# Optimization experiments

Hardware: AMD Instinct MI355X
Metric: run time of the kernel (lower is better)

## Reference

```python
import jax, jax.numpy as jnp
import numpy as np

N = 100000
E = 1600000
NFEAT = 256
NCLASS = 40
H1, C1 = 8, 8  # layer1: 8 heads x 8 channels, concat -> 64
EPS = 1e-16
NEG_SLOPE = 0.2


def setup_inputs() -> dict:
    key = jax.random.key(0)
    ks = jax.random.split(key, 10)
    x = jax.random.normal(ks[0], (N, NFEAT), dtype=jnp.float32)
    # random edges with no self-loops (PyG GATConv removes then re-adds self loops)
    src = jax.random.randint(ks[1], (E,), 0, N)
    off = jax.random.randint(ks[2], (E,), 1, N)
    dst = (src + off) % N
    edge_index = jnp.stack([src, dst]).astype(jnp.int64)
    glorot = lambda k, shp, fan: jax.random.uniform(k, shp, jnp.float32, -1.0, 1.0) * np.sqrt(6.0 / fan)
    # layer 1: in=256 -> heads=8, out=8
    W1 = glorot(ks[3], (NFEAT, H1 * C1), NFEAT + H1 * C1)
    att_src1 = glorot(ks[4], (H1, C1), 2 * C1)
    att_dst1 = glorot(ks[5], (H1, C1), 2 * C1)
    b1 = jnp.zeros((H1 * C1,), jnp.float32)
    # layer 2: in=64 -> heads=1, out=nclass
    W2 = glorot(ks[6], (H1 * C1, NCLASS), H1 * C1 + NCLASS)
    att_src2 = glorot(ks[7], (1, NCLASS), 2 * NCLASS)
    att_dst2 = glorot(ks[8], (1, NCLASS), 2 * NCLASS)
    b2 = jnp.zeros((NCLASS,), jnp.float32)
    return {"x": x, "edge_index": edge_index, "W1": W1, "att_src1": att_src1,
            "att_dst1": att_dst1, "b1": b1, "W2": W2, "att_src2": att_src2,
            "att_dst2": att_dst2, "b2": b2}


def gat_conv(x, src, dst, W, att_src, att_dst, bias, heads, out_ch):
    n = x.shape[0]
    h = (x @ W).reshape(n, heads, out_ch)               # [N,H,C]
    a_src = (h * att_src[None]).sum(-1)                  # [N,H]
    a_dst = (h * att_dst[None]).sum(-1)                  # [N,H]
    e = jax.nn.leaky_relu(a_src[src] + a_dst[dst], NEG_SLOPE)  # [E,H]
    # segment softmax over incoming edges of each target node
    m = jax.ops.segment_max(e, dst, num_segments=n)
    e = jnp.exp(e - m[dst])
    s = jax.ops.segment_sum(e, dst, num_segments=n)
    alpha = e / (s[dst] + EPS)                           # [E,H]
    msg = h[src] * alpha[..., None]                      # [E,H,C]
    out = jax.ops.segment_sum(msg, dst, num_segments=n)  # [N,H,C]
    return out.reshape(n, heads * out_ch) + bias


def reference(x, edge_index, W1, att_src1, att_dst1, b1, W2, att_src2, att_dst2, b2):
    # add self loops (PyG GATConv default add_self_loops=True)
    loops = jnp.arange(N, dtype=edge_index.dtype)
    src = jnp.concatenate([edge_index[0], loops])
    dst = jnp.concatenate([edge_index[1], loops])
    h = gat_conv(x, src, dst, W1, att_src1, att_dst1, b1, H1, C1)  # [N,64]
    h = jax.nn.elu(h)
    out = gat_conv(h, src, dst, W2, att_src2, att_dst2, b2, 1, NCLASS)  # [N,nclass]
    return out
```

## Files before the change

kernel.cpp:

```cpp
#include <hip/hip_runtime.h>
#include <hip/hip_bf16.h>

#define NN 100000
#define NE 1600000
#define NF 256
#define NC 40
#define NH 8
#define D1 64
#define NEG 0.2f
#define BSHIFT 7
#define BSZ 128
#define NB ((NN + BSZ - 1) / BSZ)
#define EPB 4096
#define NBLK ((NE + EPB - 1) / EPB)

typedef __attribute__((ext_vector_type(8))) short short8;
typedef __attribute__((ext_vector_type(4))) float f32x4;

static __device__ __forceinline__ float lrelu(float x) { return x > 0.f ? x : NEG * x; }

static __device__ __forceinline__ float2 bfx2(unsigned u) {
    union { unsigned q; float f; } a, b;
    a.q = u << 16;
    b.q = u & 0xFFFF0000u;
    return make_float2(a.f, b.f);
}

static __device__ __forceinline__ unsigned packbf2(float x, float y) {
    unsigned xu = __float_as_uint(x), yu = __float_as_uint(y);
    xu = (xu + 0x7FFFu + ((xu >> 16) & 1u)) >> 16;
    yu = (yu + 0x7FFFu + ((yu >> 16) & 1u)) >> 16;
    return xu | (yu << 16);
}

static __device__ __forceinline__ unsigned short f2b(float x) {
    unsigned u = __float_as_uint(x);
    u = (u + 0x7FFFu + ((u >> 16) & 1u)) >> 16;
    return (unsigned short)u;
}


__launch_bounds__(256)
__global__ void bhist_k(const int* __restrict__ dst, int* __restrict__ cnt) {
    __shared__ int hist[NB];
    int i = blockIdx.x, t = threadIdx.x;
    for (int b = t; b < NB; b += 256) hist[b] = 0;
    __syncthreads();
    int e0 = i * EPB;
    #pragma unroll
    for (int k = 0; k < EPB / 256; ++k) {
        int e = e0 + k * 256 + t;
        if (e < NE) atomicAdd(&hist[dst[e] >> BSHIFT], 1);
    }
    __syncthreads();
    for (int b = t; b < NB; b += 256) cnt[i * NB + b] = hist[b];
}

__launch_bounds__(256)
__global__ void bscan2_k(int* __restrict__ cnt, int* __restrict__ btot) {
    __shared__ int ps[256];
    int b = blockIdx.x, t = threadIdx.x;
    int i0 = 2 * t;
    int a = (i0 < NBLK) ? cnt[i0 * NB + b] : 0;
    int c = (i0 + 1 < NBLK) ? cnt[(i0 + 1) * NB + b] : 0;
    int s = a + c;
    ps[t] = s;
    __syncthreads();
    #pragma unroll
    for (int off = 1; off < 256; off <<= 1) {
        int x = (t >= off) ? ps[t - off] : 0;
        __syncthreads();
        ps[t] += x;
        __syncthreads();
    }
    int ex = ps[t] - s;
    if (i0 < NBLK) cnt[i0 * NB + b] = ex;
    if (i0 + 1 < NBLK) cnt[(i0 + 1) * NB + b] = ex + a;
    if (t == 255) btot[b] = ps[255];
}

__launch_bounds__(256)
__global__ void bscanB_k(const int* __restrict__ btot, int* __restrict__ bbase) {
    __shared__ int ps[256];
    int t = threadIdx.x;
    int j0 = 4 * t;
    int v[4]; int s = 0;
    #pragma unroll
    for (int k = 0; k < 4; ++k) { v[k] = (j0 + k < NB) ? btot[j0 + k] : 0; s += v[k]; }
    ps[t] = s;
    __syncthreads();
    #pragma unroll
    for (int off = 1; off < 256; off <<= 1) {
        int x = (t >= off) ? ps[t - off] : 0;
        __syncthreads();
        ps[t] += x;
        __syncthreads();
    }
    int run = ps[t] - s;
    #pragma unroll
    for (int k = 0; k < 4; ++k) { if (j0 + k < NB) bbase[j0 + k] = run; run += v[k]; }
    if (t == 0) bbase[NB] = NE;
}

__launch_bounds__(256)
__global__ void bplace_k(const int* __restrict__ src, const int* __restrict__ dst,
                         const int* __restrict__ cnt, const int* __restrict__ bbase,
                         long long* __restrict__ tmp) {
    __shared__ int loff[NB];
    int i = blockIdx.x, t = threadIdx.x;
    for (int b = t; b < NB; b += 256) loff[b] = bbase[b] + cnt[i * NB + b];
    __syncthreads();
    int e0 = i * EPB;
    #pragma unroll
    for (int k = 0; k < EPB / 256; ++k) {
        int e = e0 + k * 256 + t;
        if (e < NE) {
            int d = dst[e];
            int p = atomicAdd(&loff[d >> BSHIFT], 1);
            tmp[p] = ((long long)d << 32) | (unsigned)src[e];
        }
    }
}

__launch_bounds__(256)
__global__ void scatter2_k(const long long* __restrict__ tmp, const int* __restrict__ bbase,
                           int* __restrict__ rowptr, int* __restrict__ col) {
    __shared__ int lcnt[BSZ];
    __shared__ int lrow[BSZ];
    __shared__ int ls[BSZ];
    int b = blockIdx.x, t = threadIdx.x;
    int n0 = b << BSHIFT;
    if (t < BSZ) lcnt[t] = 0;
    __syncthreads();
    int beg = bbase[b], end = bbase[b + 1];
    for (int p = beg + t; p < end; p += 256) {
        int d = (int)(tmp[p] >> 32);
        atomicAdd(&lcnt[d - n0], 1);
    }
    __syncthreads();
    if (t < BSZ) ls[t] = lcnt[t];
    __syncthreads();
    #pragma unroll
    for (int off = 1; off < BSZ; off <<= 1) {
        int x = 0;
        if (t < BSZ && t >= off) x = ls[t - off];
        __syncthreads();
        if (t < BSZ) ls[t] += x;
        __syncthreads();
    }
    if (t < BSZ) {
        int ex = ls[t] - lcnt[t];
        lrow[t] = beg + ex;
        if (n0 + t < NN) rowptr[n0 + t] = beg + ex;
        lcnt[t] = 0;
    }
    if (b == NB - 1 && t == 0) rowptr[NN] = NE;
    __syncthreads();
    for (int p = beg + t; p < end; p += 256) {
        long long v = tmp[p];
        int d = (int)(v >> 32);
        int s = (int)(v & 0xFFFFFFFFLL);
        int o = atomicAdd(&lcnt[d - n0], 1);
        col[lrow[d - n0] + o] = s;
    }
}


__launch_bounds__(256)
__global__ void gemm1_k(const float* __restrict__ x, const float* __restrict__ W,
                        unsigned short* __restrict__ h1b) {
    __shared__ unsigned short wsw[8 * 4 * 64 * 8];
    int tid = threadIdx.x;
    int wid = tid >> 6, lane = tid & 63;
    int r0 = blockIdx.x * 128 + wid * 32;

    #pragma unroll
    for (int it = 0; it < 16; ++it) {
        int idx4 = it * 256 + tid;
        int k = idx4 >> 4;
        int c0 = (idx4 & 15) * 4;
        float4 v = *(const float4*)&W[k * 64 + c0];
        int kt = k >> 5, kg = (k >> 3) & 3, kr = k & 7;
        float vv[4] = {v.x, v.y, v.z, v.w};
        #pragma unroll
        for (int j = 0; j < 4; ++j) {
            int c = c0 + j;
            int dest = (((kt * 4 + (c >> 4)) * 64) + kg * 16 + (c & 15)) * 8 + kr;
            wsw[dest] = f2b(vv[j]);
        }
    }
    __syncthreads();

    int arow0 = r0 + (lane & 15);
    int kg8 = (lane >> 4) * 8;
    f32x4 acc[2][4] = {};
    for (int kt = 0; kt < 8; ++kt) {
        short8 af[2];
        #pragma unroll
        for (int rt = 0; rt < 2; ++rt) {
            int row = arow0 + rt * 16;
            float4 v0 = make_float4(0.f, 0.f, 0.f, 0.f), v1 = v0;
            if (row < NN) {
                const float* px = &x[row * NF + kt * 32 + kg8];
                v0 = *(const float4*)px;
                v1 = *(const float4*)(px + 4);
            }
            unsigned p0 = packbf2(v0.x, v0.y), p1 = packbf2(v0.z, v0.w);
            unsigned p2 = packbf2(v1.x, v1.y), p3 = packbf2(v1.z, v1.w);
            af[rt][0] = (short)(p0 & 0xFFFF); af[rt][1] = (short)(p0 >> 16);
            af[rt][2] = (short)(p1 & 0xFFFF); af[rt][3] = (short)(p1 >> 16);
            af[rt][4] = (short)(p2 & 0xFFFF); af[rt][5] = (short)(p2 >> 16);
            af[rt][6] = (short)(p3 & 0xFFFF); af[rt][7] = (short)(p3 >> 16);
        }
        #pragma unroll
        for (int ct = 0; ct < 4; ++ct) {
            short8 bf = *(const short8*)&wsw[((kt * 4 + ct) * 64 + lane) * 8];
            acc[0][ct] = __builtin_amdgcn_mfma_f32_16x16x32_bf16(af[0], bf, acc[0][ct], 0, 0, 0);
            acc[1][ct] = __builtin_amdgcn_mfma_f32_16x16x32_bf16(af[1], bf, acc[1][ct], 0, 0, 0);
        }
    }

    int ccol = lane & 15;
    int crow0 = r0 + (lane >> 4) * 4;
    #pragma unroll
    for (int rt = 0; rt < 2; ++rt) {
        #pragma unroll
        for (int r = 0; r < 4; ++r) {
            int grow = crow0 + rt * 16 + r;
            if (grow < NN) {
                #pragma unroll
                for (int ct = 0; ct < 4; ++ct)
                    h1b[grow * D1 + ct * 16 + ccol] = f2b(acc[rt][ct][r]);
            }
        }
    }
}


__global__ void attn1_k(const unsigned short* __restrict__ h1b, const float* __restrict__ asrc,
                        const float* __restrict__ adst,
                        float* __restrict__ as1, float* __restrict__ ad1) {
    int t = blockIdx.x * blockDim.x + threadIdx.x;
    if (t >= NN * NH) return;
    int n = t >> 3, h = t & 7;
    uint4 v = *(const uint4*)&h1b[n * D1 + h * 8];
    float hv[8];
    float2 p;
    p = bfx2(v.x); hv[0] = p.x; hv[1] = p.y;
    p = bfx2(v.y); hv[2] = p.x; hv[3] = p.y;
    p = bfx2(v.z); hv[4] = p.x; hv[5] = p.y;
    p = bfx2(v.w); hv[6] = p.x; hv[7] = p.y;
    float sa = 0.f, sd = 0.f;
    #pragma unroll
    for (int c = 0; c < 8; ++c) {
        sa = fmaf(hv[c], asrc[h * 8 + c], sa);
        sd = fmaf(hv[c], adst[h * 8 + c], sd);
    }
    as1[t] = sa;
    ad1[t] = sd;
}


__launch_bounds__(256)
__global__ void agg1_k(const unsigned short* __restrict__ h1b, const float* __restrict__ as1,
                       const float* __restrict__ ad1,
                       const int* __restrict__ rowptr, const int* __restrict__ col,
                       const float* __restrict__ b1, unsigned short* __restrict__ h1outb) {
    int n = blockIdx.x * 4 + (threadIdx.x >> 6);
    if (n >= NN) return;
    int lane = threadIdx.x & 63;
    int g = lane >> 3, ln = lane & 7;
    int row0 = rowptr[n];
    int d = rowptr[n + 1] - row0;
    float adh = ad1[n * 8 + ln];

    float acc[8] = {};
    float wsum = 0.f;
    for (int j = 0; j <= d; j += 8) {
        int jj = j + g;
        int s = (jj < d) ? col[row0 + jj] : n;
        float e = lrelu(as1[s * 8 + ln] + adh);
        float wgt = (jj <= d) ? __expf(e) : 0.f;
        wsum += wgt;
        uint4 hv = *(const uint4*)&h1b[s * D1 + ln * 8];
        float2 p;
        p = bfx2(hv.x); acc[0] = fmaf(p.x, wgt, acc[0]); acc[1] = fmaf(p.y, wgt, acc[1]);
        p = bfx2(hv.y); acc[2] = fmaf(p.x, wgt, acc[2]); acc[3] = fmaf(p.y, wgt, acc[3]);
        p = bfx2(hv.z); acc[4] = fmaf(p.x, wgt, acc[4]); acc[5] = fmaf(p.y, wgt, acc[5]);
        p = bfx2(hv.w); acc[6] = fmaf(p.x, wgt, acc[6]); acc[7] = fmaf(p.y, wgt, acc[7]);
    }
    #pragma unroll
    for (int off = 8; off <= 32; off <<= 1) {
        wsum += __shfl_xor(wsum, off, 64);
        #pragma unroll
        for (int k = 0; k < 8; ++k) acc[k] += __shfl_xor(acc[k], off, 64);
    }
    if (g == 0) {
        float inv = 1.f / (wsum + 1e-16f);
        unsigned u[4];
        #pragma unroll
        for (int k = 0; k < 4; ++k) {
            float v0 = fmaf(acc[2 * k], inv, b1[ln * 8 + 2 * k]);
            float v1 = fmaf(acc[2 * k + 1], inv, b1[ln * 8 + 2 * k + 1]);
            v0 = (v0 > 0.f) ? v0 : (__expf(v0) - 1.f);
            v1 = (v1 > 0.f) ? v1 : (__expf(v1) - 1.f);
            u[k] = packbf2(v0, v1);
        }
        uint4 w = {u[0], u[1], u[2], u[3]};
        *(uint4*)&h1outb[n * D1 + ln * 8] = w;
    }
}


__launch_bounds__(256)
__global__ void attn2_k(const unsigned short* __restrict__ h1outb, const float* __restrict__ W2,
                        const float* __restrict__ asrc, const float* __restrict__ adst,
                        float* __restrict__ as2, float* __restrict__ ad2) {
    __shared__ float w2a[64], w2d[64];
    int tid = threadIdx.x;
    if (tid < 128) {
        int c = tid & 63;
        const float* av = (tid < 64) ? asrc : adst;
        float s = 0.f;
        #pragma unroll
        for (int j = 0; j < NC; ++j) s = fmaf(W2[c * NC + j], av[j], s);
        if (tid < 64) w2a[c] = s; else w2d[c] = s;
    }
    __syncthreads();
    int n = blockIdx.x * 256 + tid;
    if (n >= NN) return;
    float sa = 0.f, sd = 0.f;
    #pragma unroll
    for (int q = 0; q < 8; ++q) {
        uint4 v = *(const uint4*)&h1outb[n * D1 + q * 8];
        int c0 = q * 8;
        float2 p;
        p = bfx2(v.x);
        sa = fmaf(p.x, w2a[c0], sa);     sd = fmaf(p.x, w2d[c0], sd);
        sa = fmaf(p.y, w2a[c0 + 1], sa); sd = fmaf(p.y, w2d[c0 + 1], sd);
        p = bfx2(v.y);
        sa = fmaf(p.x, w2a[c0 + 2], sa); sd = fmaf(p.x, w2d[c0 + 2], sd);
        sa = fmaf(p.y, w2a[c0 + 3], sa); sd = fmaf(p.y, w2d[c0 + 3], sd);
        p = bfx2(v.z);
        sa = fmaf(p.x, w2a[c0 + 4], sa); sd = fmaf(p.x, w2d[c0 + 4], sd);
        sa = fmaf(p.y, w2a[c0 + 5], sa); sd = fmaf(p.y, w2d[c0 + 5], sd);
        p = bfx2(v.w);
        sa = fmaf(p.x, w2a[c0 + 6], sa); sd = fmaf(p.x, w2d[c0 + 6], sd);
        sa = fmaf(p.y, w2a[c0 + 7], sa); sd = fmaf(p.y, w2d[c0 + 7], sd);
    }
    as2[n] = sa;
    ad2[n] = sd;
}


__launch_bounds__(256)
__global__ void agg2_k(const unsigned short* __restrict__ h1outb, const float* __restrict__ as2,
                       const float* __restrict__ ad2,
                       const int* __restrict__ rowptr, const int* __restrict__ col,
                       unsigned short* __restrict__ zb) {
    int n = blockIdx.x * 4 + (threadIdx.x >> 6);
    if (n >= NN) return;
    int lane = threadIdx.x & 63;
    int g = lane >> 3, ln = lane & 7;
    int row0 = rowptr[n];
    int d = rowptr[n + 1] - row0;
    float adn = ad2[n];

    float acc[8] = {};
    float wsum = 0.f;
    for (int j = 0; j <= d; j += 8) {
        int jj = j + g;
        int s = (jj < d) ? col[row0 + jj] : n;
        float e = lrelu(as2[s] + adn);
        float wgt = (jj <= d) ? __expf(e) : 0.f;
        wsum += wgt;
        uint4 hv = *(const uint4*)&h1outb[s * D1 + ln * 8];
        float2 p;
        p = bfx2(hv.x); acc[0] = fmaf(p.x, wgt, acc[0]); acc[1] = fmaf(p.y, wgt, acc[1]);
        p = bfx2(hv.y); acc[2] = fmaf(p.x, wgt, acc[2]); acc[3] = fmaf(p.y, wgt, acc[3]);
        p = bfx2(hv.z); acc[4] = fmaf(p.x, wgt, acc[4]); acc[5] = fmaf(p.y, wgt, acc[5]);
        p = bfx2(hv.w); acc[6] = fmaf(p.x, wgt, acc[6]); acc[7] = fmaf(p.y, wgt, acc[7]);
    }
    #pragma unroll
    for (int off = 8; off <= 32; off <<= 1) {
        wsum += __shfl_xor(wsum, off, 64);
        #pragma unroll
        for (int k = 0; k < 8; ++k) acc[k] += __shfl_xor(acc[k], off, 64);
    }
    if (g == 0) {
        float inv = 1.f / (wsum + 1e-16f);
        unsigned u[4];
        #pragma unroll
        for (int k = 0; k < 4; ++k)
            u[k] = packbf2(acc[2 * k] * inv, acc[2 * k + 1] * inv);
        uint4 w = {u[0], u[1], u[2], u[3]};
        *(uint4*)&zb[n * D1 + ln * 8] = w;
    }
}


__launch_bounds__(256)
__global__ void gemm2_k(const unsigned short* __restrict__ zb, const float* __restrict__ W2,
                        const float* __restrict__ b2, float* __restrict__ out) {
    __shared__ float xs[64 * 68];
    __shared__ float wsm[64 * 40];
    __shared__ float bs[40];
    int r0 = blockIdx.x * 64;
    int tid = threadIdx.x;
    #pragma unroll
    for (int it = 0; it < 4; ++it) {
        int idx = tid + it * 256;
        int row = idx >> 4;
        int q = (idx & 15) * 4;
        int gr = r0 + row;
        float f0 = 0.f, f1 = 0.f, f2 = 0.f, f3 = 0.f;
        if (gr < NN) {
            uint2 v = *(const uint2*)&zb[gr * D1 + q];
            float2 p0 = bfx2(v.x), p1 = bfx2(v.y);
            f0 = p0.x; f1 = p0.y; f2 = p1.x; f3 = p1.y;
        }
        xs[row * 68 + q] = f0;
        xs[row * 68 + q + 1] = f1;
        xs[row * 68 + q + 2] = f2;
        xs[row * 68 + q + 3] = f3;
    }
    #pragma unroll
    for (int it = 0; it < 10; ++it) {
        int idx = tid + it * 256;
        if (idx < 64 * 40) wsm[idx] = W2[idx];
    }
    if (tid < 40) bs[tid] = b2[tid];
    __syncthreads();
    int r = tid >> 2, q = tid & 3;
    float acc[10] = {};
    #pragma unroll 4
    for (int k = 0; k < 64; ++k) {
        float xv = xs[r * 68 + k];
        #pragma unroll
        for (int i = 0; i < 10; ++i)
            acc[i] = fmaf(xv, wsm[k * 40 + q * 10 + i], acc[i]);
    }
    int gr = r0 + r;
    if (gr < NN) {
        #pragma unroll
        for (int i = 0; i < 10; ++i) out[gr * NC + q * 10 + i] = acc[i] + bs[q * 10 + i];
    }
}


extern "C" void kernel_launch(void* const* d_in, const int* in_sizes, int n_in,
                              void* d_out, int out_size, void* d_ws, size_t ws_size,
                              hipStream_t stream) {
    const float* x = (const float*)d_in[0];
    const int* ei = (const int*)d_in[1];
    const int* src = ei;
    const int* dst = ei + NE;
    const float* W1 = (const float*)d_in[2];
    const float* asrc1 = (const float*)d_in[3];
    const float* adst1 = (const float*)d_in[4];
    const float* b1 = (const float*)d_in[5];
    const float* W2 = (const float*)d_in[6];
    const float* asrc2 = (const float*)d_in[7];
    const float* adst2 = (const float*)d_in[8];
    const float* b2 = (const float*)d_in[9];
    float* out = (float*)d_out;

    char* ws = (char*)d_ws;
    unsigned short* h1b    = (unsigned short*)(ws + 0);
    unsigned short* zb     = (unsigned short*)(ws + 0);
    float*          as1    = (float*)(ws + 12800000);
    float*          ad1    = (float*)(ws + 16000000);
    unsigned short* h1outb = (unsigned short*)(ws + 25600000);
    long long*      tmp    = (long long*)(ws + 25600000);
    float*          as2    = (float*)(ws + 38400000);
    float*          ad2    = (float*)(ws + 38800000);
    int*            col    = (int*)(ws + 39200000);
    int*            cnt    = (int*)(ws + 39200000);
    int*            rowptr = (int*)(ws + 45600000);
    int*            btot   = (int*)(ws + 46000128);
    int*            bbase  = (int*)(ws + 46003264);

    bhist_k<<<NBLK, 256, 0, stream>>>(dst, cnt);
    bscan2_k<<<NB, 256, 0, stream>>>(cnt, btot);
    bscanB_k<<<1, 256, 0, stream>>>(btot, bbase);
    bplace_k<<<NBLK, 256, 0, stream>>>(src, dst, cnt, bbase, tmp);
    scatter2_k<<<NB, 256, 0, stream>>>(tmp, bbase, rowptr, col);

    gemm1_k<<<(NN + 127) / 128, 256, 0, stream>>>(x, W1, h1b);
    attn1_k<<<(NN * NH + 255) / 256, 256, 0, stream>>>(h1b, asrc1, adst1, as1, ad1);
    agg1_k<<<(NN + 3) / 4, 256, 0, stream>>>(h1b, as1, ad1, rowptr, col, b1, h1outb);

    attn2_k<<<(NN + 255) / 256, 256, 0, stream>>>(h1outb, W2, asrc2, adst2, as2, ad2);
    agg2_k<<<(NN + 3) / 4, 256, 0, stream>>>(h1outb, as2, ad2, rowptr, col, zb);
    gemm2_k<<<(NN + 63) / 64, 256, 0, stream>>>(zb, W2, b2, out);
}
```

Before: 212.8 us.

## Fuse layer-2 attention logits into agg1, pack CSR temp, unroll gathers

Removes the separate attn2 kernel. A tiny w2pre kernel precomputes W2·att vectors, and agg1 computes the layer-2 src/dst logits from its ELU output with a shuffle reduction. The bucket temp array is packed from 64-bit to 32-bit entries (local dst in the high bits, src in 17 bits), which halves its traffic in bplace and scatter2. Both aggregation loops process two neighbors per group per iteration to raise memory-level parallelism, at the cost of more registers and an extra tiny launch.

```diff
diff --git a/kernel.cpp b/kernel.cpp
--- a/kernel.cpp
+++ b/kernel.cpp
@@ -105,7 +105,7 @@
 __launch_bounds__(256)
 __global__ void bplace_k(const int* __restrict__ src, const int* __restrict__ dst,
                          const int* __restrict__ cnt, const int* __restrict__ bbase,
-                         long long* __restrict__ tmp) {
+                         unsigned* __restrict__ tmp) {
     __shared__ int loff[NB];
     int i = blockIdx.x, t = threadIdx.x;
     for (int b = t; b < NB; b += 256) loff[b] = bbase[b] + cnt[i * NB + b];
@@ -117,13 +117,13 @@
         if (e < NE) {
             int d = dst[e];
             int p = atomicAdd(&loff[d >> BSHIFT], 1);
-            tmp[p] = ((long long)d << 32) | (unsigned)src[e];
-        }
-    }
-}
-
-__launch_bounds__(256)
-__global__ void scatter2_k(const long long* __restrict__ tmp, const int* __restrict__ bbase,
+            tmp[p] = ((unsigned)(d & 127) << 17) | (unsigned)src[e];
+        }
+    }
+}
+
+__launch_bounds__(256)
+__global__ void scatter2_k(const unsigned* __restrict__ tmp, const int* __restrict__ bbase,
                            int* __restrict__ rowptr, int* __restrict__ col) {
     __shared__ int lcnt[BSZ];
     __shared__ int lrow[BSZ];
@@ -133,10 +133,8 @@
     if (t < BSZ) lcnt[t] = 0;
     __syncthreads();
     int beg = bbase[b], end = bbase[b + 1];
-    for (int p = beg + t; p < end; p += 256) {
-        int d = (int)(tmp[p] >> 32);
-        atomicAdd(&lcnt[d - n0], 1);
-    }
+    for (int p = beg + t; p < end; p += 256)
+        atomicAdd(&lcnt[tmp[p] >> 17], 1);
     __syncthreads();
     if (t < BSZ) ls[t] = lcnt[t];
     __syncthreads();
@@ -157,11 +155,11 @@
     if (b == NB - 1 && t == 0) rowptr[NN] = NE;
     __syncthreads();
     for (int p = beg + t; p < end; p += 256) {
-        long long v = tmp[p];
-        int d = (int)(v >> 32);
-        int s = (int)(v & 0xFFFFFFFFLL);
-        int o = atomicAdd(&lcnt[d - n0], 1);
-        col[lrow[d - n0] + o] = s;
+        unsigned v = tmp[p];
+        int dloc = v >> 17;
+        int s = (int)(v & 0x1FFFFu);
+        int o = atomicAdd(&lcnt[dloc], 1);
+        col[lrow[dloc] + o] = s;
     }
 }
 
@@ -261,11 +259,26 @@
 }
 
 
+__launch_bounds__(128)
+__global__ void w2pre_k(const float* __restrict__ W2, const float* __restrict__ asrc,
+                        const float* __restrict__ adst, float* __restrict__ w2vec) {
+    int t = threadIdx.x;
+    int c = t & 63;
+    const float* av = (t < 64) ? asrc : adst;
+    float s = 0.f;
+    #pragma unroll
+    for (int j = 0; j < NC; ++j) s = fmaf(W2[c * NC + j], av[j], s);
+    w2vec[t] = s;
+}
+
+
 __launch_bounds__(256)
 __global__ void agg1_k(const unsigned short* __restrict__ h1b, const float* __restrict__ as1,
                        const float* __restrict__ ad1,
                        const int* __restrict__ rowptr, const int* __restrict__ col,
-                       const float* __restrict__ b1, unsigned short* __restrict__ h1outb) {
+                       const float* __restrict__ b1, const float* __restrict__ w2vec,
+                       unsigned short* __restrict__ h1outb,
+                       float* __restrict__ as2, float* __restrict__ ad2) {
     int n = blockIdx.x * 4 + (threadIdx.x >> 6);
     if (n >= NN) return;
     int lane = threadIdx.x & 63;
@@ -276,18 +289,26 @@
 
     float acc[8] = {};
     float wsum = 0.f;
-    for (int j = 0; j <= d; j += 8) {
-        int jj = j + g;
-        int s = (jj < d) ? col[row0 + jj] : n;
-        float e = lrelu(as1[s * 8 + ln] + adh);
-        float wgt = (jj <= d) ? __expf(e) : 0.f;
-        wsum += wgt;
-        uint4 hv = *(const uint4*)&h1b[s * D1 + ln * 8];
+    for (int j = 0; j <= d; j += 16) {
+        int jA = j + g, jB = j + 8 + g;
+        bool vA = (jA <= d), vB = (jB <= d);
+        int sA = (jA < d) ? col[row0 + jA] : n;
+        int sB = (jB < d) ? col[row0 + jB] : n;
+        float wA = vA ? __expf(lrelu(as1[sA * 8 + ln] + adh)) : 0.f;
+        float wB = vB ? __expf(lrelu(as1[sB * 8 + ln] + adh)) : 0.f;
+        uint4 hA = vA ? *(const uint4*)&h1b[sA * D1 + ln * 8] : make_uint4(0, 0, 0, 0);
+        uint4 hB = vB ? *(const uint4*)&h1b[sB * D1 + ln * 8] : make_uint4(0, 0, 0, 0);
         float2 p;
-        p = bfx2(hv.x); acc[0] = fmaf(p.x, wgt, acc[0]); acc[1] = fmaf(p.y, wgt, acc[1]);
-        p = bfx2(hv.y); acc[2] = fmaf(p.x, wgt, acc[2]); acc[3] = fmaf(p.y, wgt, acc[3]);
-        p = bfx2(hv.z); acc[4] = fmaf(p.x, wgt, acc[4]); acc[5] = fmaf(p.y, wgt, acc[5]);
-        p = bfx2(hv.w); acc[6] = fmaf(p.x, wgt, acc[6]); acc[7] = fmaf(p.y, wgt, acc[7]);
+        wsum += wA;
+        p = bfx2(hA.x); acc[0] = fmaf(p.x, wA, acc[0]); acc[1] = fmaf(p.y, wA, acc[1]);
+        p = bfx2(hA.y); acc[2] = fmaf(p.x, wA, acc[2]); acc[3] = fmaf(p.y, wA, acc[3]);
+        p = bfx2(hA.z); acc[4] = fmaf(p.x, wA, acc[4]); acc[5] = fmaf(p.y, wA, acc[5]);
+        p = bfx2(hA.w); acc[6] = fmaf(p.x, wA, acc[6]); acc[7] = fmaf(p.y, wA, acc[7]);
+        wsum += wB;
+        p = bfx2(hB.x); acc[0] = fmaf(p.x, wB, acc[0]); acc[1] = fmaf(p.y, wB, acc[1]);
+        p = bfx2(hB.y); acc[2] = fmaf(p.x, wB, acc[2]); acc[3] = fmaf(p.y, wB, acc[3]);
+        p = bfx2(hB.z); acc[4] = fmaf(p.x, wB, acc[4]); acc[5] = fmaf(p.y, wB, acc[5]);
+        p = bfx2(hB.w); acc[6] = fmaf(p.x, wB, acc[6]); acc[7] = fmaf(p.y, wB, acc[7]);
     }
     #pragma unroll
     for (int off = 8; off <= 32; off <<= 1) {
@@ -297,59 +318,27 @@
     }
     if (g == 0) {
         float inv = 1.f / (wsum + 1e-16f);
+        float vals[8];
+        #pragma unroll
+        for (int k = 0; k < 8; ++k) {
+            float v = fmaf(acc[k], inv, b1[ln * 8 + k]);
+            vals[k] = (v > 0.f) ? v : (__expf(v) - 1.f);
+        }
         unsigned u[4];
         #pragma unroll
-        for (int k = 0; k < 4; ++k) {
-            float v0 = fmaf(acc[2 * k], inv, b1[ln * 8 + 2 * k]);
-            float v1 = fmaf(acc[2 * k + 1], inv, b1[ln * 8 + 2 * k + 1]);
-            v0 = (v0 > 0.f) ? v0 : (__expf(v0) - 1.f);
-            v1 = (v1 > 0.f) ? v1 : (__expf(v1) - 1.f);
-            u[k] = packbf2(v0, v1);
-        }
+        for (int k = 0; k < 4; ++k) u[k] = packbf2(vals[2 * k], vals[2 * k + 1]);
         uint4 w = {u[0], u[1], u[2], u[3]};
         *(uint4*)&h1outb[n * D1 + ln * 8] = w;
-    }
-}
-
-
-__launch_bounds__(256)
-__global__ void attn2_k(const unsigned short* __restrict__ h1outb, const float* __restrict__ W2,
-                        const float* __restrict__ asrc, const float* __restrict__ adst,
-                        float* __restrict__ as2, float* __restrict__ ad2) {
-    __shared__ float w2a[64], w2d[64];
-    int tid = threadIdx.x;
-    if (tid < 128) {
-        int c = tid & 63;
-        const float* av = (tid < 64) ? asrc : adst;
-        float s = 0.f;
-        #pragma unroll
-        for (int j = 0; j < NC; ++j) s = fmaf(W2[c * NC + j], av[j], s);
-        if (tid < 64) w2a[c] = s; else w2d[c] = s;
-    }
-    __syncthreads();
-    int n = blockIdx.x * 256 + tid;
-    if (n >= NN) return;
-    float sa = 0.f, sd = 0.f;
-    #pragma unroll
-    for (int q = 0; q < 8; ++q) {
-        uint4 v = *(const uint4*)&h1outb[n * D1 + q * 8];
-        int c0 = q * 8;
-        float2 p;
-        p = bfx2(v.x);
-        sa = fmaf(p.x, w2a[c0], sa);     sd = fmaf(p.x, w2d[c0], sd);
-        sa = fmaf(p.y, w2a[c0 + 1], sa); sd = fmaf(p.y, w2d[c0 + 1], sd);
-        p = bfx2(v.y);
-        sa = fmaf(p.x, w2a[c0 + 2], sa); sd = fmaf(p.x, w2d[c0 + 2], sd);
-        sa = fmaf(p.y, w2a[c0 + 3], sa); sd = fmaf(p.y, w2d[c0 + 3], sd);
-        p = bfx2(v.z);
-        sa = fmaf(p.x, w2a[c0 + 4], sa); sd = fmaf(p.x, w2d[c0 + 4], sd);
-        sa = fmaf(p.y, w2a[c0 + 5], sa); sd = fmaf(p.y, w2d[c0 + 5], sd);
-        p = bfx2(v.w);
-        sa = fmaf(p.x, w2a[c0 + 6], sa); sd = fmaf(p.x, w2d[c0 + 6], sd);
-        sa = fmaf(p.y, w2a[c0 + 7], sa); sd = fmaf(p.y, w2d[c0 + 7], sd);
-    }
-    as2[n] = sa;
-    ad2[n] = sd;
+        float pa = 0.f, pd = 0.f;
+        #pragma unroll
+        for (int k = 0; k < 8; ++k) {
+            pa = fmaf(vals[k], w2vec[ln * 8 + k], pa);
+            pd = fmaf(vals[k], w2vec[64 + ln * 8 + k], pd);
+        }
+        pa += __shfl_xor(pa, 1); pa += __shfl_xor(pa, 2); pa += __shfl_xor(pa, 4);
+        pd += __shfl_xor(pd, 1); pd += __shfl_xor(pd, 2); pd += __shfl_xor(pd, 4);
+        if (ln == 0) { as2[n] = pa; ad2[n] = pd; }
+    }
 }
 
 
@@ -368,18 +357,26 @@
 
     float acc[8] = {};
     float wsum = 0.f;
-    for (int j = 0; j <= d; j += 8) {
-        int jj = j + g;
-        int s = (jj < d) ? col[row0 + jj] : n;
-        float e = lrelu(as2[s] + adn);
-        float wgt = (jj <= d) ? __expf(e) : 0.f;
-        wsum += wgt;
-        uint4 hv = *(const uint4*)&h1outb[s * D1 + ln * 8];
+    for (int j = 0; j <= d; j += 16) {
+        int jA = j + g, jB = j + 8 + g;
+        bool vA = (jA <= d), vB = (jB <= d);
+        int sA = (jA < d) ? col[row0 + jA] : n;
+        int sB = (jB < d) ? col[row0 + jB] : n;
+        float wA = vA ? __expf(lrelu(as2[sA] + adn)) : 0.f;
+        float wB = vB ? __expf(lrelu(as2[sB] + adn)) : 0.f;
+        uint4 hA = vA ? *(const uint4*)&h1outb[sA * D1 + ln * 8] : make_uint4(0, 0, 0, 0);
+        uint4 hB = vB ? *(const uint4*)&h1outb[sB * D1 + ln * 8] : make_uint4(0, 0, 0, 0);
         float2 p;
-        p = bfx2(hv.x); acc[0] = fmaf(p.x, wgt, acc[0]); acc[1] = fmaf(p.y, wgt, acc[1]);
-        p = bfx2(hv.y); acc[2] = fmaf(p.x, wgt, acc[2]); acc[3] = fmaf(p.y, wgt, acc[3]);
-        p = bfx2(hv.z); acc[4] = fmaf(p.x, wgt, acc[4]); acc[5] = fmaf(p.y, wgt, acc[5]);
-        p = bfx2(hv.w); acc[6] = fmaf(p.x, wgt, acc[6]); acc[7] = fmaf(p.y, wgt, acc[7]);
+        wsum += wA;
+        p = bfx2(hA.x); acc[0] = fmaf(p.x, wA, acc[0]); acc[1] = fmaf(p.y, wA, acc[1]);
+        p = bfx2(hA.y); acc[2] = fmaf(p.x, wA, acc[2]); acc[3] = fmaf(p.y, wA, acc[3]);
+        p = bfx2(hA.z); acc[4] = fmaf(p.x, wA, acc[4]); acc[5] = fmaf(p.y, wA, acc[5]);
+        p = bfx2(hA.w); acc[6] = fmaf(p.x, wA, acc[6]); acc[7] = fmaf(p.y, wA, acc[7]);
+        wsum += wB;
+        p = bfx2(hB.x); acc[0] = fmaf(p.x, wB, acc[0]); acc[1] = fmaf(p.y, wB, acc[1]);
+        p = bfx2(hB.y); acc[2] = fmaf(p.x, wB, acc[2]); acc[3] = fmaf(p.y, wB, acc[3]);
+        p = bfx2(hB.z); acc[4] = fmaf(p.x, wB, acc[4]); acc[5] = fmaf(p.y, wB, acc[5]);
+        p = bfx2(hB.w); acc[6] = fmaf(p.x, wB, acc[6]); acc[7] = fmaf(p.y, wB, acc[7]);
     }
     #pragma unroll
     for (int off = 8; off <= 32; off <<= 1) {
@@ -471,7 +468,7 @@
     float*          as1    = (float*)(ws + 12800000);
     float*          ad1    = (float*)(ws + 16000000);
     unsigned short* h1outb = (unsigned short*)(ws + 25600000);
-    long long*      tmp    = (long long*)(ws + 25600000);
+    unsigned*       tmp    = (unsigned*)(ws + 25600000);
     float*          as2    = (float*)(ws + 38400000);
     float*          ad2    = (float*)(ws + 38800000);
     int*            col    = (int*)(ws + 39200000);
@@ -479,6 +476,7 @@
     int*            rowptr = (int*)(ws + 45600000);
     int*            btot   = (int*)(ws + 46000128);
     int*            bbase  = (int*)(ws + 46003264);
+    float*          w2vec  = (float*)(ws + 46006400);
 
     bhist_k<<<NBLK, 256, 0, stream>>>(dst, cnt);
     bscan2_k<<<NB, 256, 0, stream>>>(cnt, btot);
@@ -488,9 +486,10 @@
 
     gemm1_k<<<(NN + 127) / 128, 256, 0, stream>>>(x, W1, h1b);
     attn1_k<<<(NN * NH + 255) / 256, 256, 0, stream>>>(h1b, asrc1, adst1, as1, ad1);
-    agg1_k<<<(NN + 3) / 4, 256, 0, stream>>>(h1b, as1, ad1, rowptr, col, b1, h1outb);
-
-    attn2_k<<<(NN + 255) / 256, 256, 0, stream>>>(h1outb, W2, asrc2, adst2, as2, ad2);
+    w2pre_k<<<1, 128, 0, stream>>>(W2, asrc2, adst2, w2vec);
+    agg1_k<<<(NN + 3) / 4, 256, 0, stream>>>(h1b, as1, ad1, rowptr, col, b1, w2vec,
+                                             h1outb, as2, ad2);
+
     agg2_k<<<(NN + 3) / 4, 256, 0, stream>>>(h1outb, as2, ad2, rowptr, col, zb);
     gemm2_k<<<(NN + 63) / 64, 256, 0, stream>>>(zb, W2, b2, out);
 }
```

Measured after the change: 226.0 us. 1.06x slower.
